# Optimization experiments

Measured on AMD Instinct MI355X. Metric: run time of the kernel, lower is better.

The kernel has to match this reference:

```python
import jax, jax.numpy as jnp
import numpy as np

B, T = 2, 2048
D_MODEL = 1024
N_LAYERS = 2
VOCAB = 256
BLOCK = 2048
LOCAL = 128
STRIDE = 256
NHEAD = D_MODEL // 64  # 16
HEAD_DIM = D_MODEL // NHEAD  # 64
LN_EPS = 1e-5


def setup_inputs() -> dict:
    key = jax.random.key(0)
    ks = jax.random.split(key, 16)
    L, d = N_LAYERS, D_MODEL

    def g(k, shape, scale=0.02):
        return (jax.random.normal(k, shape, dtype=jnp.float32) * scale)

    return {
        "x": jax.random.randint(ks[0], (B, T), 0, VOCAB),
        "embed": g(ks[1], (VOCAB, d)),
        "pos_embed": g(ks[2], (BLOCK, d)),
        # per-layer weights stacked on leading L axis; Linear as y = x @ W + b
        "Wq": g(ks[3], (L, d, d)), "bq": jnp.zeros((L, d), jnp.float32),
        "Wk": g(ks[4], (L, d, d)), "bk": jnp.zeros((L, d), jnp.float32),
        "Wv": g(ks[5], (L, d, d)), "bv": jnp.zeros((L, d), jnp.float32),
        "Wo": g(ks[6], (L, d, d)), "bo": jnp.zeros((L, d), jnp.float32),
        "g1": jnp.ones((L, d), jnp.float32), "be1": jnp.zeros((L, d), jnp.float32),
        "W1": g(ks[7], (L, d, 4 * d)), "bf1": jnp.zeros((L, 4 * d), jnp.float32),
        "W2": g(ks[8], (L, 4 * d, d)), "bf2": jnp.zeros((L, d), jnp.float32),
        "g2": jnp.ones((L, d), jnp.float32), "be2": jnp.zeros((L, d), jnp.float32),
        "gf": jnp.ones((d,), jnp.float32), "bef": jnp.zeros((d,), jnp.float32),
        "Whead": g(ks[9], (d, VOCAB)),
    }


def _ln(x, gamma, beta):
    mu = jnp.mean(x, axis=-1, keepdims=True)
    var = jnp.mean(jnp.square(x - mu), axis=-1, keepdims=True)
    return (x - mu) * jax.lax.rsqrt(var + LN_EPS) * gamma + beta


def _sparse_mask(t):
    # allowed[i, j] = True if token i may attend to token j
    i = jnp.arange(t)[:, None]
    j = jnp.arange(t)[None, :]
    causal = j <= i
    local = (i - j) <= LOCAL
    glob = (j % STRIDE) == 0
    return causal & (local | glob)


def _sparse_attn(q, k, v, allowed):
    # q, k, v: [B, T, D] -> [B, H, T, hd]
    b, t, d = q.shape
    def split(x):
        return x.reshape(b, t, NHEAD, HEAD_DIM).transpose(0, 2, 1, 3)
    q, k, v = split(q), split(k), split(v)
    scale = HEAD_DIM ** -0.5
    scores = jnp.einsum("bhqd,bhkd->bhqk", q, k) * scale
    scores = jnp.where(allowed[None, None], scores, -jnp.inf)
    attn = jax.nn.softmax(scores, axis=-1)  # every row has j=i allowed -> no NaN
    out = jnp.einsum("bhqk,bhkd->bhqd", attn, v)
    return out.transpose(0, 2, 1, 3).reshape(b, t, d)


def reference(x, embed, pos_embed, Wq, bq, Wk, bk, Wv, bv, Wo, bo,
              g1, be1, W1, bf1, W2, bf2, g2, be2, gf, bef, Whead):
    b, t = x.shape
    h = embed[x] + pos_embed[jnp.arange(t)][None]
    allowed = _sparse_mask(t)
    for l in range(N_LAYERS):
        h_n = _ln(h, g1[l], be1[l])
        q = h_n @ Wq[l] + bq[l]
        k = h_n @ Wk[l] + bk[l]
        v = h_n @ Wv[l] + bv[l]
        attn_out = _sparse_attn(q, k, v, allowed)
        h = h + (attn_out @ Wo[l] + bo[l])
        h2 = _ln(h, g2[l], be2[l])
        ffn = jax.nn.gelu(h2 @ W1[l] + bf1[l], approximate=False) @ W2[l] + bf2[l]
        h = h + ffn
    h = _ln(h, gf, bef)
    return h @ Whead
```

## Files before the change

kernel.cpp:

```cpp
#include <hip/hip_runtime.h>
#include <hip/hip_bf16.h>

#define BB 2
#define TT 2048
#define DD 1024
#define FF 4096
#define VV 256
#define HH 16
#define HD 64
#define MM (BB * TT)
#define LOCAL_W 128
#define STRIDE_G 256
#define QS 3072

typedef short s16x8 __attribute__((ext_vector_type(8)));
typedef __bf16 bf16x8 __attribute__((ext_vector_type(8)));
typedef float f32x4 __attribute__((ext_vector_type(4)));

#define WAITVM(N) asm volatile("s_waitcnt vmcnt(" #N ")" ::: "memory")

__device__ __forceinline__ float b2f(unsigned short u) {
  return __builtin_bit_cast(float, (unsigned int)u << 16);
}
__device__ __forceinline__ unsigned short f2b(float f) {
  __hip_bfloat16 h = __float2bfloat16(f);
  return __builtin_bit_cast(unsigned short, h);
}
__device__ __forceinline__ void gl_lds16(const unsigned short* g, unsigned short* l) {
  __builtin_amdgcn_global_load_lds(
      (const __attribute__((address_space(1))) void*)g,
      (__attribute__((address_space(3))) void*)l, 16, 0, 0);
}

__global__ __launch_bounds__(256) void transpose_k(const float* __restrict__ W,
                                                   unsigned short* __restrict__ WT,
                                                   int K, int N) {
  __shared__ float t[32][33];
  const int n0 = blockIdx.x * 32, k0 = blockIdx.y * 32;
  const int tx = threadIdx.x, ty = threadIdx.y;
  for (int r = ty; r < 32; r += 8) t[r][tx] = W[(size_t)(k0 + r) * N + n0 + tx];
  __syncthreads();
  for (int r = ty; r < 32; r += 8)
    WT[(size_t)(n0 + r) * K + k0 + tx] = f2b(t[tx][r]);
}

__global__ __launch_bounds__(256) void concat_bias(const float* __restrict__ bq,
                                                   const float* __restrict__ bk,
                                                   const float* __restrict__ bv,
                                                   float* __restrict__ bcat) {
  const int i = blockIdx.x * 256 + threadIdx.x;
  const int l = i / QS, j = i - l * QS;
  float v;
  if (j < DD) v = bq[l * DD + j];
  else if (j < 2 * DD) v = bk[l * DD + j - DD];
  else v = bv[l * DD + j - 2 * DD];
  bcat[i] = v;
}

__global__ __launch_bounds__(256) void embed_kernel(const int* __restrict__ x,
                                                    const float* __restrict__ emb,
                                                    const float* __restrict__ pos,
                                                    float* __restrict__ h) {
  const int row = blockIdx.x;
  const int c = threadIdx.x * 4;
  const int tok = x[row];
  const int t = row & (TT - 1);
  float4 e = *(const float4*)&emb[(size_t)tok * DD + c];
  float4 p = *(const float4*)&pos[(size_t)t * DD + c];
  e.x += p.x; e.y += p.y; e.z += p.z; e.w += p.w;
  *(float4*)&h[(size_t)row * DD + c] = e;
}

__global__ __launch_bounds__(256) void ln_kernel(const float* __restrict__ x,
                                                 const float* __restrict__ g,
                                                 const float* __restrict__ be,
                                                 unsigned short* __restrict__ out) {
  const int row = blockIdx.x;
  const int tid = threadIdx.x;
  const float4 v = *(const float4*)&x[(size_t)row * DD + tid * 4];
  float s = v.x + v.y + v.z + v.w;
  float sq = v.x * v.x + v.y * v.y + v.z * v.z + v.w * v.w;
#pragma unroll
  for (int off = 32; off; off >>= 1) {
    s += __shfl_xor(s, off);
    sq += __shfl_xor(sq, off);
  }
  __shared__ float ss[4], ssq[4];
  const int w = tid >> 6, lane = tid & 63;
  if (lane == 0) { ss[w] = s; ssq[w] = sq; }
  __syncthreads();
  s = ss[0] + ss[1] + ss[2] + ss[3];
  sq = ssq[0] + ssq[1] + ssq[2] + ssq[3];
  const float mean = s * (1.0f / DD);
  const float var = sq * (1.0f / DD) - mean * mean;
  const float rstd = rsqrtf(var + 1e-5f);
  const float4 gv = *(const float4*)&g[tid * 4];
  const float4 bv = *(const float4*)&be[tid * 4];
  ushort4 o;
  o.x = f2b((v.x - mean) * rstd * gv.x + bv.x);
  o.y = f2b((v.y - mean) * rstd * gv.y + bv.y);
  o.z = f2b((v.z - mean) * rstd * gv.z + bv.z);
  o.w = f2b((v.w - mean) * rstd * gv.w + bv.w);
  *(ushort4*)&out[(size_t)row * DD + tid * 4] = o;
}

template <int BIG, int EPI>
__global__ __launch_bounds__(512, 2) void gemm_p(const unsigned short* __restrict__ A,
                                                 const unsigned short* __restrict__ BT,
                                                 const float* __restrict__ bias,
                                                 const float* __restrict__ res,
                                                 void* __restrict__ outp,
                                                 int M, int N, int K, int nbx, int nwg2,
                                                 int ksub) {
  constexpr int BM = BIG ? 256 : 128;
  constexpr int MF = BIG ? 8 : 4;
  constexpr int NF = BIG ? 4 : 2;
  __shared__ __align__(16) unsigned short lds[4][BM * 64];
  const int tid = threadIdx.x;
  const int lane = tid & 63;
  const int w = tid >> 6;
  const int nwg = gridDim.x;
  const int orig = blockIdx.x;
  const int wg = (orig & 7) * (nwg >> 3) + (orig >> 3);
  const int ks = wg / nwg2;
  const int rem = wg - ks * nwg2;
  const int n0 = (rem % nbx) * BM;
  const int m0 = (rem / nbx) * BM;
  const int kb = ks * ksub;
  const int wm = w >> 2, wn = w & 3;
  f32x4 acc[MF][NF] = {};

  auto STAGE = [&](int t) {
    const int b = t & 3;
    const int kt = kb + (t << 5);
#pragma unroll
    for (int i = 0; i < (BIG ? 2 : 1); i++) {
      const int s = tid + (i << 9);
      const int row = s >> 2, sc = s & 3;
      const int c = sc ^ ((row >> 1) & 3);
      gl_lds16(&A[(size_t)(m0 + row) * K + kt + c * 8], &lds[b][s * 8]);
      gl_lds16(&BT[(size_t)(n0 + row) * K + kt + c * 8], &lds[b][BM * 32 + s * 8]);
    }
  };

  const int NT = ksub >> 5;
  STAGE(0); STAGE(1); STAGE(2);

  for (int t = 0; t < NT; ++t) {
    const int ahead = NT - 1 - t;
    if (BIG) {
      if (ahead >= 2) WAITVM(8); else if (ahead == 1) WAITVM(4); else WAITVM(0);
    } else {
      if (ahead >= 2) WAITVM(4); else if (ahead == 1) WAITVM(2); else WAITVM(0);
    }
    __builtin_amdgcn_s_barrier();
    asm volatile("" ::: "memory");
    if (t + 3 < NT) STAGE(t + 3);
    const int b = t & 3;
    const int rA = lane & 15, cr = lane >> 4;
    bf16x8 af[MF], bfr[NF];
#pragma unroll
    for (int m = 0; m < MF; m++) {
      const int row = wm * (BM / 2) + m * 16 + rA;
      af[m] = __builtin_bit_cast(
          bf16x8, *(const s16x8*)&lds[b][row * 32 + ((cr ^ ((row >> 1) & 3)) << 3)]);
    }
#pragma unroll
    for (int n = 0; n < NF; n++) {
      const int row = wn * (BM / 4) + n * 16 + rA;
      bfr[n] = __builtin_bit_cast(
          bf16x8, *(const s16x8*)&lds[b][BM * 32 + row * 32 + ((cr ^ ((row >> 1) & 3)) << 3)]);
    }
    __builtin_amdgcn_s_setprio(1);
#pragma unroll
    for (int m = 0; m < MF; m++)
#pragma unroll
      for (int n = 0; n < NF; n++)
        acc[m][n] = __builtin_amdgcn_mfma_f32_16x16x32_bf16(af[m], bfr[n], acc[m][n], 0, 0, 0);
    __builtin_amdgcn_s_setprio(0);
  }

  const int r0 = (lane >> 4) * 4;
  const int cc = lane & 15;
  float* pout = (EPI == 0) ? ((float*)outp + (size_t)ks * M * N) : (float*)outp;
#pragma unroll
  for (int m = 0; m < MF; m++) {
#pragma unroll
    for (int n = 0; n < NF; n++) {
#pragma unroll
      for (int r = 0; r < 4; r++) {
        const int row = m0 + wm * (BM / 2) + m * 16 + r0 + r;
        const int col = n0 + wn * (BM / 4) + n * 16 + cc;
        const size_t idx = (size_t)row * N + col;
        if (EPI == 0) {
          pout[idx] = acc[m][n][r];
        } else {
          float val = acc[m][n][r] + bias[col];
          if (EPI == 1) {
            ((unsigned short*)outp)[idx] = f2b(val);
          } else if (EPI == 2) {
            ((float*)outp)[idx] = val + res[idx];
          } else {
            const float gv = 0.5f * val * (1.0f + erff(val * 0.70710678118654752f));
            ((unsigned short*)outp)[idx] = f2b(gv);
          }
        }
      }
    }
  }
}

template <int NP, bool BIAS, bool RES>
__global__ __launch_bounds__(256) void reduce_k(float* __restrict__ dst,
                                                const float* __restrict__ parts,
                                                const float* __restrict__ bias,
                                                int ncols, size_t total) {
  const size_t i = ((size_t)blockIdx.x * 256 + threadIdx.x) * 4;
  if (i >= total) return;
  f32x4 acc = {};
  if (RES) acc = *(const f32x4*)&dst[i];
  if (BIAS) {
    const int col = (int)(i % ncols);
    acc += *(const f32x4*)&bias[col];
  }
#pragma unroll
  for (int p = 0; p < NP; p++) acc += *(const f32x4*)&parts[(size_t)p * total + i];
  *(f32x4*)&dst[i] = acc;
}

#define QT 16
#define KT 32
#define NTMAX 6
#define KP 72
#define PP 40

__global__ __launch_bounds__(256) void attn_mfma(const unsigned short* __restrict__ qkv,
                                                 unsigned short* __restrict__ outg) {
  __shared__ __align__(16) unsigned short kvs[4][KT * KP];
  __shared__ __align__(16) unsigned short pls[4][QT * PP];
  const int tid = threadIdx.x;
  const int wid = tid >> 6, lane = tid & 63;
  const int qgrp = blockIdx.x & 31;
  const int bh = blockIdx.x >> 5;
  const int h = bh & (HH - 1), b = bh >> 4;
  const size_t baseq = (size_t)b * TT * QS + (size_t)h * HD;
  const size_t baseo = (size_t)b * TT * DD + (size_t)h * HD;
  const int i0 = qgrp * 64 + wid * 16;
  const int g = lane >> 4;
  const int c = lane & 15;

  const int i0b = qgrp * 64 + 48;
  const int ka0b = (i0b > 128) ? ((i0b - 128) & ~31) : 0;
  const int nlb = ((i0b + 16 - ka0b) + 31) >> 5;
  const int neb = (ka0b + 255) >> 8;
  const int ka0 = (i0 > 128) ? ((i0 - 128) & ~31) : 0;
  const int ne = (ka0 + 255) >> 8;

  const s16x8 qf0 = *(const s16x8*)&qkv[baseq + (size_t)(i0 + c) * QS + g * 8];
  const s16x8 qf1 = *(const s16x8*)&qkv[baseq + (size_t)(i0 + c) * QS + 32 + g * 8];

  f32x4 sc[NTMAX][2];
  float smax[4] = {-1e30f, -1e30f, -1e30f, -1e30f};

#pragma unroll
  for (int t = 0; t < NTMAX; t++) {
    if (t > nlb) continue;
    const bool isg = (t == 0);
    if (isg && neb == 0) continue;
    const int kt0 = ka0 + (t - 1) * 32;
#pragma unroll
    for (int it = 0; it < 4; it++) {
      const int row = it * 8 + (lane >> 3);
      const int ch = lane & 7;
      const int j = isg ? ((row < ne) ? row * STRIDE_G : 0) : (kt0 + row);
      *(s16x8*)&kvs[wid][row * KP + ch * 8] =
          *(const s16x8*)&qkv[baseq + DD + (size_t)j * QS + ch * 8];
    }
    __syncthreads();
#pragma unroll
    for (int half = 0; half < 2; half++) {
      const int key = half * 16 + c;
      const bf16x8 kb0 = __builtin_bit_cast(bf16x8, *(const s16x8*)&kvs[wid][key * KP + g * 8]);
      const bf16x8 kb1 = __builtin_bit_cast(bf16x8, *(const s16x8*)&kvs[wid][key * KP + 32 + g * 8]);
      f32x4 a = {};
      a = __builtin_amdgcn_mfma_f32_16x16x32_bf16(__builtin_bit_cast(bf16x8, qf0), kb0, a, 0, 0, 0);
      a = __builtin_amdgcn_mfma_f32_16x16x32_bf16(__builtin_bit_cast(bf16x8, qf1), kb1, a, 0, 0, 0);
#pragma unroll
      for (int r = 0; r < 4; r++) {
        const int i = i0 + g * 4 + r;
        bool ok;
        if (isg) {
          ok = (key < ne);
        } else {
          const int j = kt0 + key;
          ok = (j <= i) && (((i - j) <= LOCAL_W) || ((j & (STRIDE_G - 1)) == 0));
        }
        const float s = ok ? a[r] * 0.125f : -1e30f;
        sc[t][half][r] = s;
        smax[r] = fmaxf(smax[r], s);
      }
    }
    __syncthreads();
  }
#pragma unroll
  for (int r = 0; r < 4; r++)
#pragma unroll
    for (int off = 8; off; off >>= 1)
      smax[r] = fmaxf(smax[r], __shfl_xor(smax[r], off));

  f32x4 o[4] = {};
  float lsum[4] = {0.f, 0.f, 0.f, 0.f};
#pragma unroll
  for (int t = 0; t < NTMAX; t++) {
    if (t > nlb) continue;
    const bool isg = (t == 0);
    if (isg && neb == 0) continue;
    const int kt0 = ka0 + (t - 1) * 32;
#pragma unroll
    for (int it = 0; it < 4; it++) {
      const int row = it * 8 + (lane >> 3);
      const int ch = lane & 7;
      const int j = isg ? ((row < ne) ? row * STRIDE_G : 0) : (kt0 + row);
      *(s16x8*)&kvs[wid][row * KP + ch * 8] =
          *(const s16x8*)&qkv[baseq + 2 * DD + (size_t)j * QS + ch * 8];
    }
#pragma unroll
    for (int half = 0; half < 2; half++)
#pragma unroll
      for (int r = 0; r < 4; r++) {
        const float p = __expf(sc[t][half][r] - smax[r]);
        lsum[r] += p;
        pls[wid][(g * 4 + r) * PP + half * 16 + c] = f2b(p);
      }
    __syncthreads();
    const bf16x8 pa = __builtin_bit_cast(bf16x8, *(const s16x8*)&pls[wid][c * PP + g * 8]);
#pragma unroll
    for (int d0 = 0; d0 < 4; d0++) {
      s16x8 bv;
#pragma unroll
      for (int e = 0; e < 8; e++)
        bv[e] = (short)kvs[wid][(g * 8 + e) * KP + d0 * 16 + c];
      o[d0] = __builtin_amdgcn_mfma_f32_16x16x32_bf16(pa, __builtin_bit_cast(bf16x8, bv), o[d0], 0, 0, 0);
    }
    __syncthreads();
  }
#pragma unroll
  for (int r = 0; r < 4; r++)
#pragma unroll
    for (int off = 8; off; off >>= 1)
      lsum[r] += __shfl_xor(lsum[r], off);
#pragma unroll
  for (int d0 = 0; d0 < 4; d0++)
#pragma unroll
    for (int r = 0; r < 4; r++)
      outg[baseo + (size_t)(i0 + g * 4 + r) * DD + d0 * 16 + c] = f2b(o[d0][r] / lsum[r]);
}

extern "C" void kernel_launch(void* const* d_in, const int* in_sizes, int n_in,
                              void* d_out, int out_size, void* d_ws, size_t ws_size,
                              hipStream_t stream) {
  const int* x = (const int*)d_in[0];
  const float* embed = (const float*)d_in[1];
  const float* pos = (const float*)d_in[2];
  const float* Wq = (const float*)d_in[3];
  const float* bq = (const float*)d_in[4];
  const float* Wk = (const float*)d_in[5];
  const float* bk = (const float*)d_in[6];
  const float* Wv = (const float*)d_in[7];
  const float* bv = (const float*)d_in[8];
  const float* Wo = (const float*)d_in[9];
  const float* bo = (const float*)d_in[10];
  const float* g1 = (const float*)d_in[11];
  const float* be1 = (const float*)d_in[12];
  const float* W1 = (const float*)d_in[13];
  const float* bf1 = (const float*)d_in[14];
  const float* W2 = (const float*)d_in[15];
  const float* bf2 = (const float*)d_in[16];
  const float* g2 = (const float*)d_in[17];
  const float* be2 = (const float*)d_in[18];
  const float* gf = (const float*)d_in[19];
  const float* bef = (const float*)d_in[20];
  const float* Whead = (const float*)d_in[21];

  char* ws = (char*)d_ws;
  size_t off = 0;
  auto alloc = [&](size_t bytes) -> void* {
    void* p = ws + off;
    off += (bytes + 255) & ~(size_t)255;
    return p;
  };
  unsigned short* WqkvT = (unsigned short*)alloc((size_t)2 * QS * DD * 2);
  unsigned short* WoT = (unsigned short*)alloc((size_t)2 * DD * DD * 2);
  unsigned short* W1T = (unsigned short*)alloc((size_t)2 * DD * FF * 2);
  unsigned short* W2T = (unsigned short*)alloc((size_t)2 * DD * FF * 2);
  unsigned short* WheadT = (unsigned short*)alloc((size_t)DD * VV * 2);
  float* bcat = (float*)alloc((size_t)2 * QS * 4);
  float* h = (float*)alloc((size_t)MM * DD * 4);
  unsigned short* hn = (unsigned short*)alloc((size_t)MM * DD * 2);
  unsigned short* qkvb = (unsigned short*)alloc((size_t)MM * QS * 2);
  unsigned short* attnb = (unsigned short*)alloc((size_t)MM * DD * 2);
  unsigned short* mid = (unsigned short*)alloc((size_t)MM * FF * 2);
  float* ffn2p = (float*)qkvb;
  float* headp = (float*)mid;
  (void)ws_size;

  const dim3 tb(32, 8);
  for (int l = 0; l < 2; l++) {
    const size_t wo = (size_t)l * DD * DD;
    const size_t wf = (size_t)l * DD * FF;
    transpose_k<<<dim3(DD / 32, DD / 32), tb, 0, stream>>>(Wq + wo, WqkvT + (size_t)l * QS * DD, DD, DD);
    transpose_k<<<dim3(DD / 32, DD / 32), tb, 0, stream>>>(Wk + wo, WqkvT + ((size_t)l * QS + DD) * DD, DD, DD);
    transpose_k<<<dim3(DD / 32, DD / 32), tb, 0, stream>>>(Wv + wo, WqkvT + ((size_t)l * QS + 2 * DD) * DD, DD, DD);
    transpose_k<<<dim3(DD / 32, DD / 32), tb, 0, stream>>>(Wo + wo, WoT + wo, DD, DD);
    transpose_k<<<dim3(FF / 32, DD / 32), tb, 0, stream>>>(W1 + wf, W1T + wf, DD, FF);
    transpose_k<<<dim3(DD / 32, FF / 32), tb, 0, stream>>>(W2 + wf, W2T + wf, FF, DD);
  }
  transpose_k<<<dim3(VV / 32, DD / 32), tb, 0, stream>>>(Whead, WheadT, DD, VV);
  concat_bias<<<24, 256, 0, stream>>>(bq, bk, bv, bcat);

  embed_kernel<<<MM, 256, 0, stream>>>(x, embed, pos, h);

  for (int l = 0; l < 2; l++) {
    const size_t wo = (size_t)l * DD * DD;
    const size_t wf = (size_t)l * DD * FF;
    ln_kernel<<<MM, 256, 0, stream>>>(h, g1 + l * DD, be1 + l * DD, hn);
    gemm_p<1, 1><<<(QS / 256) * (MM / 256), 512, 0, stream>>>(
        hn, WqkvT + (size_t)l * QS * DD, bcat + l * QS, nullptr, qkvb,
        MM, QS, DD, QS / 256, (QS / 256) * (MM / 256), DD);
    attn_mfma<<<BB * HH * (TT / 64), 256, 0, stream>>>(qkvb, attnb);
    gemm_p<0, 2><<<(DD / 128) * (MM / 128), 512, 0, stream>>>(
        attnb, WoT + wo, bo + l * DD, h, h,
        MM, DD, DD, DD / 128, (DD / 128) * (MM / 128), DD);
    ln_kernel<<<MM, 256, 0, stream>>>(h, g2 + l * DD, be2 + l * DD, hn);
    gemm_p<1, 3><<<(FF / 256) * (MM / 256), 512, 0, stream>>>(
        hn, W1T + wf, bf1 + l * FF, nullptr, mid,
        MM, FF, DD, FF / 256, (FF / 256) * (MM / 256), DD);
    gemm_p<0, 0><<<2 * (DD / 128) * (MM / 128), 512, 0, stream>>>(
        mid, W2T + wf, nullptr, nullptr, ffn2p,
        MM, DD, FF, DD / 128, (DD / 128) * (MM / 128), FF / 2);
    reduce_k<2, true, true><<<(MM * DD) / 1024, 256, 0, stream>>>(
        h, ffn2p, bf2 + l * DD, DD, (size_t)MM * DD);
  }
  ln_kernel<<<MM, 256, 0, stream>>>(h, gf, bef, hn);
  gemm_p<0, 0><<<4 * (VV / 128) * (MM / 128), 512, 0, stream>>>(
      hn, WheadT, nullptr, nullptr, headp,
      MM, VV, DD, VV / 128, (VV / 128) * (MM / 128), DD / 4);
  reduce_k<4, false, false><<<(MM * VV) / 1024, 256, 0, stream>>>(
      (float*)d_out, headp, nullptr, VV, (size_t)MM * VV);
}
```

Before: 472.3 us.

## Add 256x256 double-buffered BK=64 GEMM kernel for QKV and FFN1

Introduces gemm8p, a 256x256 tile GEMM with K-step 64, two LDS buffers (128KB), 8-way XOR swizzle, and a schedule that interleaves A-fragment loads with MFMA sub-phases separated by barriers and sched_barrier. It replaces the BIG variant of gemm_p for the QKV and W1+GELU projections, and gemm_p is simplified to the 128-tile path only. The aim is to overlap global-to-LDS prefetch of the next K-block with the current compute and cut per-iteration barrier overhead. The cost is more barriers inside each tile, and 128KB of LDS per workgroup may limit occupancy below the declared launch bound of 2.

```diff
diff --git a/kernel.cpp b/kernel.cpp
--- a/kernel.cpp
+++ b/kernel.cpp
@@ -30,6 +30,9 @@
   __builtin_amdgcn_global_load_lds(
       (const __attribute__((address_space(1))) void*)g,
       (__attribute__((address_space(3))) void*)l, 16, 0, 0);
+}
+__device__ __forceinline__ bf16x8 ldsr(const unsigned short* p) {
+  return __builtin_bit_cast(bf16x8, *(const s16x8*)p);
 }
 
 __global__ __launch_bounds__(256) void transpose_k(const float* __restrict__ W,
@@ -104,7 +107,134 @@
   *(ushort4*)&out[(size_t)row * DD + tid * 4] = o;
 }
 
-template <int BIG, int EPI>
+template <int EPI>
+__global__ __launch_bounds__(512, 2) void gemm8p(const unsigned short* __restrict__ A,
+                                                 const unsigned short* __restrict__ BT,
+                                                 const float* __restrict__ bias,
+                                                 unsigned short* __restrict__ outp,
+                                                 int M, int N, int K, int nbx) {
+  __shared__ __align__(16) unsigned short lds[65536];
+  const int tid = threadIdx.x;
+  const int lane = tid & 63;
+  const int w = tid >> 6;
+  const int nwg = gridDim.x;
+  const int orig = blockIdx.x;
+  const int wg = (orig & 7) * (nwg >> 3) + (orig >> 3);
+  const int n0 = (wg % nbx) * 256, m0 = (wg / nbx) * 256;
+  const int wm = w >> 2, wn = w & 3;
+  f32x4 acc[8][4] = {};
+
+  const unsigned short* aSrc[4];
+  const unsigned short* bSrc[4];
+  int dstOff[4];
+#pragma unroll
+  for (int i = 0; i < 4; i++) {
+    const int s = tid + (i << 9);
+    const int row = s >> 3, c = s & 7;
+    const int l = c ^ (row & 7);
+    aSrc[i] = &A[(size_t)(m0 + row) * K + l * 8];
+    bSrc[i] = &BT[(size_t)(n0 + row) * K + l * 8];
+    dstOff[i] = s * 8;
+  }
+  auto STAGE = [&](int tb, int buf) {
+    const int kt = tb << 6;
+    const int bb = buf << 15;
+#pragma unroll
+    for (int i = 0; i < 4; i++) gl_lds16(aSrc[i] + kt, &lds[bb + dstOff[i]]);
+#pragma unroll
+    for (int i = 0; i < 4; i++) gl_lds16(bSrc[i] + kt, &lds[bb + 16384 + dstOff[i]]);
+  };
+
+  const int rA = lane & 15, cr = lane >> 4;
+  const int pch = (cr ^ (rA & 7)) << 3;
+  const int aIdx0 = (wm * 128 + rA) * 64 + pch;
+  const int bIdx0 = 16384 + (wn * 64 + rA) * 64 + pch;
+
+  auto TILE = [&](const int buf, const int tb, const bool pref) {
+    const int bb = buf << 15;
+    bf16x8 bfr[4][2];
+    if (pref) STAGE(tb + 1, buf ^ 1);
+#pragma unroll
+    for (int n = 0; n < 4; n++)
+#pragma unroll
+      for (int ks = 0; ks < 2; ks++)
+        bfr[n][ks] = ldsr(&lds[(bIdx0 + bb + n * 1024) ^ (ks << 5)]);
+    {
+      bf16x8 af[2][2];
+#pragma unroll
+      for (int mm = 0; mm < 2; mm++)
+#pragma unroll
+        for (int ks = 0; ks < 2; ks++)
+          af[mm][ks] = ldsr(&lds[(aIdx0 + bb + mm * 1024) ^ (ks << 5)]);
+      __builtin_amdgcn_s_barrier();
+      asm volatile("s_waitcnt lgkmcnt(0)" ::: "memory");
+      __builtin_amdgcn_sched_barrier(0);
+      __builtin_amdgcn_s_setprio(1);
+#pragma unroll
+      for (int mm = 0; mm < 2; mm++)
+#pragma unroll
+        for (int n = 0; n < 4; n++)
+#pragma unroll
+          for (int ks = 0; ks < 2; ks++)
+            acc[mm][n] = __builtin_amdgcn_mfma_f32_16x16x32_bf16(af[mm][ks], bfr[n][ks],
+                                                                 acc[mm][n], 0, 0, 0);
+      __builtin_amdgcn_s_setprio(0);
+      __builtin_amdgcn_s_barrier();
+    }
+#pragma unroll
+    for (int q = 1; q < 4; q++) {
+      bf16x8 af[2][2];
+#pragma unroll
+      for (int mm = 0; mm < 2; mm++)
+#pragma unroll
+        for (int ks = 0; ks < 2; ks++)
+          af[mm][ks] = ldsr(&lds[(aIdx0 + bb + (q * 2 + mm) * 1024) ^ (ks << 5)]);
+      if (q == 3) WAITVM(0);
+      __builtin_amdgcn_s_barrier();
+      asm volatile("s_waitcnt lgkmcnt(0)" ::: "memory");
+      __builtin_amdgcn_sched_barrier(0);
+      __builtin_amdgcn_s_setprio(1);
+#pragma unroll
+      for (int mm = 0; mm < 2; mm++)
+#pragma unroll
+        for (int n = 0; n < 4; n++)
+#pragma unroll
+          for (int ks = 0; ks < 2; ks++)
+            acc[q * 2 + mm][n] = __builtin_amdgcn_mfma_f32_16x16x32_bf16(
+                af[mm][ks], bfr[n][ks], acc[q * 2 + mm][n], 0, 0, 0);
+      __builtin_amdgcn_s_setprio(0);
+      __builtin_amdgcn_s_barrier();
+    }
+  };
+
+  const int NT = K >> 6;
+  STAGE(0, 0);
+  WAITVM(0);
+  __builtin_amdgcn_s_barrier();
+  for (int it = 0; it < NT; it += 2) {
+    TILE(0, it, it + 1 < NT);
+    TILE(1, it + 1, it + 2 < NT);
+  }
+
+  const int r0 = (lane >> 4) * 4;
+  const int cc = lane & 15;
+#pragma unroll
+  for (int m = 0; m < 8; m++) {
+#pragma unroll
+    for (int n = 0; n < 4; n++) {
+#pragma unroll
+      for (int r = 0; r < 4; r++) {
+        const int row = m0 + wm * 128 + m * 16 + r0 + r;
+        const int col = n0 + wn * 64 + n * 16 + cc;
+        float val = acc[m][n][r] + bias[col];
+        if (EPI == 3) val = 0.5f * val * (1.0f + erff(val * 0.70710678118654752f));
+        outp[(size_t)row * N + col] = f2b(val);
+      }
+    }
+  }
+}
+
+template <int EPI>
 __global__ __launch_bounds__(512, 2) void gemm_p(const unsigned short* __restrict__ A,
                                                  const unsigned short* __restrict__ BT,
                                                  const float* __restrict__ bias,
@@ -112,9 +242,7 @@
                                                  void* __restrict__ outp,
                                                  int M, int N, int K, int nbx, int nwg2,
                                                  int ksub) {
-  constexpr int BM = BIG ? 256 : 128;
-  constexpr int MF = BIG ? 8 : 4;
-  constexpr int NF = BIG ? 4 : 2;
+  constexpr int BM = 128;
   __shared__ __align__(16) unsigned short lds[4][BM * 64];
   const int tid = threadIdx.x;
   const int lane = tid & 63;
@@ -128,19 +256,16 @@
   const int m0 = (rem / nbx) * BM;
   const int kb = ks * ksub;
   const int wm = w >> 2, wn = w & 3;
-  f32x4 acc[MF][NF] = {};
+  f32x4 acc[4][2] = {};
 
   auto STAGE = [&](int t) {
     const int b = t & 3;
     const int kt = kb + (t << 5);
-#pragma unroll
-    for (int i = 0; i < (BIG ? 2 : 1); i++) {
-      const int s = tid + (i << 9);
-      const int row = s >> 2, sc = s & 3;
-      const int c = sc ^ ((row >> 1) & 3);
-      gl_lds16(&A[(size_t)(m0 + row) * K + kt + c * 8], &lds[b][s * 8]);
-      gl_lds16(&BT[(size_t)(n0 + row) * K + kt + c * 8], &lds[b][BM * 32 + s * 8]);
-    }
+    const int s = tid;
+    const int row = s >> 2, sc = s & 3;
+    const int c = sc ^ ((row >> 1) & 3);
+    gl_lds16(&A[(size_t)(m0 + row) * K + kt + c * 8], &lds[b][s * 8]);
+    gl_lds16(&BT[(size_t)(n0 + row) * K + kt + c * 8], &lds[b][BM * 32 + s * 8]);
   };
 
   const int NT = ksub >> 5;
@@ -148,34 +273,28 @@
 
   for (int t = 0; t < NT; ++t) {
     const int ahead = NT - 1 - t;
-    if (BIG) {
-      if (ahead >= 2) WAITVM(8); else if (ahead == 1) WAITVM(4); else WAITVM(0);
-    } else {
-      if (ahead >= 2) WAITVM(4); else if (ahead == 1) WAITVM(2); else WAITVM(0);
-    }
+    if (ahead >= 2) WAITVM(4); else if (ahead == 1) WAITVM(2); else WAITVM(0);
     __builtin_amdgcn_s_barrier();
     asm volatile("" ::: "memory");
     if (t + 3 < NT) STAGE(t + 3);
     const int b = t & 3;
     const int rA = lane & 15, cr = lane >> 4;
-    bf16x8 af[MF], bfr[NF];
-#pragma unroll
-    for (int m = 0; m < MF; m++) {
-      const int row = wm * (BM / 2) + m * 16 + rA;
-      af[m] = __builtin_bit_cast(
-          bf16x8, *(const s16x8*)&lds[b][row * 32 + ((cr ^ ((row >> 1) & 3)) << 3)]);
-    }
-#pragma unroll
-    for (int n = 0; n < NF; n++) {
-      const int row = wn * (BM / 4) + n * 16 + rA;
-      bfr[n] = __builtin_bit_cast(
-          bf16x8, *(const s16x8*)&lds[b][BM * 32 + row * 32 + ((cr ^ ((row >> 1) & 3)) << 3)]);
+    bf16x8 af[4], bfr[2];
+#pragma unroll
+    for (int m = 0; m < 4; m++) {
+      const int row = wm * 64 + m * 16 + rA;
+      af[m] = ldsr(&lds[b][row * 32 + ((cr ^ ((row >> 1) & 3)) << 3)]);
+    }
+#pragma unroll
+    for (int n = 0; n < 2; n++) {
+      const int row = wn * 32 + n * 16 + rA;
+      bfr[n] = ldsr(&lds[b][BM * 32 + row * 32 + ((cr ^ ((row >> 1) & 3)) << 3)]);
     }
     __builtin_amdgcn_s_setprio(1);
 #pragma unroll
-    for (int m = 0; m < MF; m++)
-#pragma unroll
-      for (int n = 0; n < NF; n++)
+    for (int m = 0; m < 4; m++)
+#pragma unroll
+      for (int n = 0; n < 2; n++)
         acc[m][n] = __builtin_amdgcn_mfma_f32_16x16x32_bf16(af[m], bfr[n], acc[m][n], 0, 0, 0);
     __builtin_amdgcn_s_setprio(0);
   }
@@ -184,26 +303,18 @@
   const int cc = lane & 15;
   float* pout = (EPI == 0) ? ((float*)outp + (size_t)ks * M * N) : (float*)outp;
 #pragma unroll
-  for (int m = 0; m < MF; m++) {
-#pragma unroll
-    for (int n = 0; n < NF; n++) {
+  for (int m = 0; m < 4; m++) {
+#pragma unroll
+    for (int n = 0; n < 2; n++) {
 #pragma unroll
       for (int r = 0; r < 4; r++) {
-        const int row = m0 + wm * (BM / 2) + m * 16 + r0 + r;
-        const int col = n0 + wn * (BM / 4) + n * 16 + cc;
+        const int row = m0 + wm * 64 + m * 16 + r0 + r;
+        const int col = n0 + wn * 32 + n * 16 + cc;
         const size_t idx = (size_t)row * N + col;
         if (EPI == 0) {
           pout[idx] = acc[m][n][r];
         } else {
-          float val = acc[m][n][r] + bias[col];
-          if (EPI == 1) {
-            ((unsigned short*)outp)[idx] = f2b(val);
-          } else if (EPI == 2) {
-            ((float*)outp)[idx] = val + res[idx];
-          } else {
-            const float gv = 0.5f * val * (1.0f + erff(val * 0.70710678118654752f));
-            ((unsigned short*)outp)[idx] = f2b(gv);
-          }
+          ((float*)outp)[idx] = acc[m][n][r] + bias[col] + res[idx];
         }
       }
     }
@@ -424,25 +535,23 @@
     const size_t wo = (size_t)l * DD * DD;
     const size_t wf = (size_t)l * DD * FF;
     ln_kernel<<<MM, 256, 0, stream>>>(h, g1 + l * DD, be1 + l * DD, hn);
-    gemm_p<1, 1><<<(QS / 256) * (MM / 256), 512, 0, stream>>>(
-        hn, WqkvT + (size_t)l * QS * DD, bcat + l * QS, nullptr, qkvb,
-        MM, QS, DD, QS / 256, (QS / 256) * (MM / 256), DD);
+    gemm8p<1><<<(QS / 256) * (MM / 256), 512, 0, stream>>>(
+        hn, WqkvT + (size_t)l * QS * DD, bcat + l * QS, qkvb, MM, QS, DD, QS / 256);
     attn_mfma<<<BB * HH * (TT / 64), 256, 0, stream>>>(qkvb, attnb);
-    gemm_p<0, 2><<<(DD / 128) * (MM / 128), 512, 0, stream>>>(
+    gemm_p<2><<<(DD / 128) * (MM / 128), 512, 0, stream>>>(
         attnb, WoT + wo, bo + l * DD, h, h,
         MM, DD, DD, DD / 128, (DD / 128) * (MM / 128), DD);
     ln_kernel<<<MM, 256, 0, stream>>>(h, g2 + l * DD, be2 + l * DD, hn);
-    gemm_p<1, 3><<<(FF / 256) * (MM / 256), 512, 0, stream>>>(
-        hn, W1T + wf, bf1 + l * FF, nullptr, mid,
-        MM, FF, DD, FF / 256, (FF / 256) * (MM / 256), DD);
-    gemm_p<0, 0><<<2 * (DD / 128) * (MM / 128), 512, 0, stream>>>(
+    gemm8p<3><<<(FF / 256) * (MM / 256), 512, 0, stream>>>(
+        hn, W1T + wf, bf1 + l * FF, mid, MM, FF, DD, FF / 256);
+    gemm_p<0><<<2 * (DD / 128) * (MM / 128), 512, 0, stream>>>(
         mid, W2T + wf, nullptr, nullptr, ffn2p,
         MM, DD, FF, DD / 128, (DD / 128) * (MM / 128), FF / 2);
     reduce_k<2, true, true><<<(MM * DD) / 1024, 256, 0, stream>>>(
         h, ffn2p, bf2 + l * DD, DD, (size_t)MM * DD);
   }
   ln_kernel<<<MM, 256, 0, stream>>>(h, gf, bef, hn);
-  gemm_p<0, 0><<<4 * (VV / 128) * (MM / 128), 512, 0, stream>>>(
+  gemm_p<0><<<4 * (VV / 128) * (MM / 128), 512, 0, stream>>>(
       hn, WheadT, nullptr, nullptr, headp,
       MM, VV, DD, VV / 128, (VV / 128) * (MM / 128), DD / 4);
   reduce_k<4, false, false><<<(MM * VV) / 1024, 256, 0, stream>>>(
```

After: 477.3 us. No clear change (+1.1%).
